# Optimization experiments

Measured on AMD Instinct MI355X. Metric: run time of the kernel, lower is better.

## Reference

```python
import jax, jax.numpy as jnp
import numpy as np

N = 50000      # num_nodes
E = 400000     # num_edges
HDIM = 256     # h_dim
H = 4          # num_heads
D = HDIM // H  # per-head dim
NEG_SLOPE = 0.2  # DGL GATConv default leaky-relu slope


def setup_inputs() -> dict:
    key = jax.random.key(0)
    ks = jax.random.split(key, 12)
    sw = 1.0 / np.sqrt(HDIM)   # fan-in scaling for fc weights
    sa = 1.0 / np.sqrt(D)      # scaling for attention vectors
    return {
        "nids": jnp.arange(N, dtype=jnp.int32),
        "edge_src": jax.random.randint(ks[0], (E,), 0, N, dtype=jnp.int32),
        "edge_dst": jax.random.randint(ks[1], (E,), 0, N, dtype=jnp.int32),
        "emb": jax.random.normal(ks[2], (N, HDIM), jnp.float32),
        "W1": jax.random.normal(ks[3], (HDIM, HDIM), jnp.float32) * sw,
        "al1": jax.random.normal(ks[4], (H, D), jnp.float32) * sa,
        "ar1": jax.random.normal(ks[5], (H, D), jnp.float32) * sa,
        "b1": jnp.zeros((HDIM,), jnp.float32),
        "W2": jax.random.normal(ks[6], (HDIM, HDIM), jnp.float32) * sw,
        "al2": jax.random.normal(ks[7], (H, D), jnp.float32) * sa,
        "ar2": jax.random.normal(ks[8], (H, D), jnp.float32) * sa,
        "b2": jnp.zeros((HDIM,), jnp.float32),
    }


def _gat_layer(x, src, dst, W, al, ar, b):
    # DGL GATConv: fc -> per-head attn logits -> edge softmax over dst -> scatter-add
    f = (x @ W).reshape(-1, H, D)                       # [N,H,D]
    el = jnp.einsum('nhd,hd->nh', f, al)                # [N,H]
    er = jnp.einsum('nhd,hd->nh', f, ar)                # [N,H]
    e = jax.nn.leaky_relu(el[src] + er[dst], NEG_SLOPE) # [E,H]
    # segment softmax over incoming edges of each dst node
    m = jax.ops.segment_max(e, dst, num_segments=N)     # [N,H] (-inf for empty)
    ex = jnp.exp(e - m[dst])                            # [E,H]
    s = jax.ops.segment_sum(ex, dst, num_segments=N)    # [N,H]
    alpha = ex / s[dst]                                 # [E,H]
    msg = alpha[:, :, None] * f[src]                    # [E,H,D]
    out = jax.ops.segment_sum(msg, dst, num_segments=N) # [N,H,D]
    return out + b.reshape(1, H, D)


def reference(nids, edge_src, edge_dst, emb, W1, al1, ar1, b1, W2, al2, ar2, b2):
    x = emb[nids]                                        # embedding lookup [N,HDIM]
    h = _gat_layer(x, edge_src, edge_dst, W1, al1, ar1, b1)  # [N,H,D]
    h = jax.nn.elu(h)
    h = h.reshape(-1, HDIM)                              # concat heads for layer 2
    out = _gat_layer(h, edge_src, edge_dst, W2, al2, ar2, b2)  # [N,H,D]
    return out  # dropout is identity at inference
```

## Files before the change

kernel.cpp:

```cpp
#include <hip/hip_runtime.h>
#include <math.h>

#define NN 50000
#define EE 400000
#define HD 256
#define NH 4
#define DH 64
#define NEG_SLOPE 0.2f
#define NTILES 3125

typedef __attribute__((ext_vector_type(8))) _Float16 f16x8;
typedef __attribute__((ext_vector_type(4))) float f32x4;

__device__ __forceinline__ float bf2f(unsigned short h) {
  return __uint_as_float(((unsigned)h) << 16);
}

__global__ void k_zero_i32(int* __restrict__ p, int n) {
  int i = blockIdx.x * blockDim.x + threadIdx.x;
  if (i < n) p[i] = 0;
}

__global__ void k_count(const int* __restrict__ dst, int* __restrict__ counts,
                        int* __restrict__ rank) {
  int e = blockIdx.x * blockDim.x + threadIdx.x;
  if (e < EE) rank[e] = atomicAdd(&counts[dst[e]], 1);
}

__global__ void k_scan1(const int* __restrict__ counts, int* __restrict__ row_ptr,
                        int* __restrict__ bsums) {
  __shared__ int sm[256];
  int i = blockIdx.x * 256 + threadIdx.x;
  int v = (i < NN) ? counts[i] : 0;
  sm[threadIdx.x] = v;
  __syncthreads();
  for (int off = 1; off < 256; off <<= 1) {
    int t = (threadIdx.x >= off) ? sm[threadIdx.x - off] : 0;
    __syncthreads();
    sm[threadIdx.x] += t;
    __syncthreads();
  }
  if (i < NN) row_ptr[i + 1] = sm[threadIdx.x];
  if (threadIdx.x == 255) bsums[blockIdx.x] = sm[255];
}

__global__ void k_scan2(int* __restrict__ bsums, int nb) {
  __shared__ int sm[256];
  int v = (threadIdx.x < nb) ? bsums[threadIdx.x] : 0;
  sm[threadIdx.x] = v;
  __syncthreads();
  for (int off = 1; off < 256; off <<= 1) {
    int t = (threadIdx.x >= off) ? sm[threadIdx.x - off] : 0;
    __syncthreads();
    sm[threadIdx.x] += t;
    __syncthreads();
  }
  if (threadIdx.x < nb) bsums[threadIdx.x] = sm[threadIdx.x] - v;
}

__global__ void k_scan3(int* __restrict__ row_ptr, const int* __restrict__ bsums) {
  int i = blockIdx.x * 256 + threadIdx.x;
  if (i < NN) row_ptr[i + 1] += bsums[blockIdx.x];
  if (blockIdx.x == 0 && threadIdx.x == 0) row_ptr[0] = 0;
}

__global__ void k_scatter(const int* __restrict__ src, const int* __restrict__ dst,
                          const int* __restrict__ row_ptr, const int* __restrict__ rank,
                          int* __restrict__ csr_src) {
  int e = blockIdx.x * blockDim.x + threadIdx.x;
  if (e < EE) csr_src[row_ptr[dst[e]] + rank[e]] = src[e];
}

__global__ __launch_bounds__(256) void k_prep_w2(const float* __restrict__ W1,
                                                 const float* __restrict__ W2,
                                                 _Float16* __restrict__ W1t,
                                                 _Float16* __restrict__ W2t) {
  int b = blockIdx.x;
  const float* W = (b < 256) ? W1 : W2;
  _Float16* Wt = (b < 256) ? W1t : W2t;
  int t = (b & 255) * 256 + threadIdx.x;
  int n = t & 255, k = t >> 8;
  float x = W[(size_t)k * 256 + n];
  size_t o = (size_t)(k >> 5) * 8192 + (size_t)((k >> 3) & 3) * 2048 + (size_t)n * 8 + (k & 7);
  Wt[o] = (_Float16)x;
}

__device__ __forceinline__ void gload_lds16(const void* g, void* l) {
  __builtin_amdgcn_global_load_lds((const __attribute__((address_space(1))) void*)g,
                                   (__attribute__((address_space(3))) void*)l, 16, 0, 0);
}

__global__ __launch_bounds__(768, 3) void k_gemm_mfma(
    const float* __restrict__ A, const int* __restrict__ idx,
    const _Float16* __restrict__ Wt,
    const float* __restrict__ al, const float* __restrict__ ar,
    __bf16* __restrict__ C, float* __restrict__ el, float* __restrict__ er) {
  __shared__ f16x8 Bs[8192];

  int tid = threadIdx.x;
  int lane = tid & 63;
  int w = tid >> 6;
  int khalf = lane >> 4;
  int l15 = lane & 15;

  for (int i = tid; i < 8192; i += 768)
    gload_lds16(Wt + (size_t)i * 8, (void*)&Bs[i]);

  float alv[16], arv[16];
#pragma unroll
  for (int nf = 0; nf < 16; ++nf) {
    alv[nf] = al[nf * 16 + l15];
    arv[nf] = ar[nf * 16 + l15];
  }

  int nt = 1;
  int tiles[2];
  tiles[0] = blockIdx.x * 12 + w;
  int t2 = 3072 + blockIdx.x;
  if (w == 0 && t2 < NTILES) { tiles[1] = t2; nt = 2; }

  __syncthreads();

  for (int it = 0; it < nt; ++it) {
    int t = tiles[it];
    int row = t * 16 + l15;
    int arow = idx ? idx[row] : row;
    const float* ap = A + (size_t)arow * HD + khalf * 8;

    f32x4 acc[16];
#pragma unroll
    for (int nf = 0; nf < 16; ++nf) acc[nf] = (f32x4){0.f, 0.f, 0.f, 0.f};

#pragma unroll 2
    for (int kb = 0; kb < 8; ++kb) {
      float xx[8];
      *(float4*)&xx[0] = *(const float4*)(ap + kb * 32);
      *(float4*)&xx[4] = *(const float4*)(ap + kb * 32 + 4);
      f16x8 ah, alo;
#pragma unroll
      for (int i = 0; i < 8; ++i) {
        _Float16 h = (_Float16)xx[i];
        ah[i] = h;
        alo[i] = (_Float16)(xx[i] - (float)h);
      }
#pragma unroll
      for (int nf = 0; nf < 16; ++nf) {
        f16x8 bv = Bs[kb * 1024 + khalf * 256 + nf * 16 + l15];
        acc[nf] = __builtin_amdgcn_mfma_f32_16x16x32_f16(ah, bv, acc[nf], 0, 0, 0);
        acc[nf] = __builtin_amdgcn_mfma_f32_16x16x32_f16(alo, bv, acc[nf], 0, 0, 0);
      }
    }

    int rowbase = t * 16 + khalf * 4;
#pragma unroll
    for (int r = 0; r < 4; ++r) {
      int row_ = rowbase + r;
      float seh[4], srh[4];
#pragma unroll
      for (int h = 0; h < 4; ++h) {
        float s1 = 0.f, s2 = 0.f;
#pragma unroll
        for (int j = 0; j < 4; ++j) {
          int nf = h * 4 + j;
          float v = acc[nf][r];
          s1 = fmaf(v, alv[nf], s1);
          s2 = fmaf(v, arv[nf], s2);
          C[(size_t)row_ * HD + nf * 16 + l15] = (__bf16)v;
        }
#pragma unroll
        for (int off = 1; off < 16; off <<= 1) {
          s1 += __shfl_xor(s1, off);
          s2 += __shfl_xor(s2, off);
        }
        seh[h] = s1;
        srh[h] = s2;
      }
      if (l15 == 0) {
        *(float4*)&el[row_ * NH] = make_float4(seh[0], seh[1], seh[2], seh[3]);
        *(float4*)&er[row_ * NH] = make_float4(srh[0], srh[1], srh[2], srh[3]);
      }
    }
  }
}

__global__ __launch_bounds__(256) void k_aggregate(const __bf16* __restrict__ f,
                                                   const float* __restrict__ el,
                                                   const float* __restrict__ er,
                                                   const int* __restrict__ row_ptr,
                                                   const int* __restrict__ csr_src,
                                                   const float* __restrict__ bias,
                                                   float* __restrict__ out, int act) {
  int node = blockIdx.x * 4 + (threadIdx.x >> 6);
  if (node >= NN) return;
  int lane = threadIdx.x & 63;
  int start = row_ptr[node];
  int deg = row_ptr[node + 1] - start;

  float ern = er[node * NH + (lane & 3)];

  int sreg[4];
  float ereg[4];
  float mloc = -INFINITY;
#pragma unroll
  for (int c = 0; c < 4; ++c) {
    int j = c * 16 + (lane >> 2);
    int s = 0;
    float e = -INFINITY;
    if (c * 16 < deg && j < deg) {
      s = csr_src[start + j];
      e = el[s * NH + (lane & 3)] + ern;
      e = (e >= 0.f) ? e : NEG_SLOPE * e;
    }
    sreg[c] = s;
    ereg[c] = e;
    mloc = fmaxf(mloc, e);
  }
  for (int j0 = 64; j0 < deg; j0 += 16) {
    int j = j0 + (lane >> 2);
    if (j < deg) {
      int s = csr_src[start + j];
      float e = el[s * NH + (lane & 3)] + ern;
      e = (e >= 0.f) ? e : NEG_SLOPE * e;
      mloc = fmaxf(mloc, e);
    }
  }
  float mm = mloc;
#pragma unroll
  for (int off = 4; off < 64; off <<= 1) mm = fmaxf(mm, __shfl_xor(mm, off));

  float vreg[4];
  float vloc = 0.f;
#pragma unroll
  for (int c = 0; c < 4; ++c) {
    float v = (ereg[c] > -INFINITY) ? __expf(ereg[c] - mm) : 0.f;
    vreg[c] = v;
    vloc += v;
  }
  for (int j0 = 64; j0 < deg; j0 += 16) {
    int j = j0 + (lane >> 2);
    if (j < deg) {
      int s = csr_src[start + j];
      float e = el[s * NH + (lane & 3)] + ern;
      e = (e >= 0.f) ? e : NEG_SLOPE * e;
      vloc += __expf(e - mm);
    }
  }
  float ss = vloc;
#pragma unroll
  for (int off = 4; off < 64; off <<= 1) ss += __shfl_xor(ss, off);

  float inv_own = (ss > 0.f) ? (1.f / ss) : 0.f;
  float areg[4];
#pragma unroll
  for (int c = 0; c < 4; ++c) areg[c] = vreg[c] * inv_own;

  int head = lane >> 4;

  float4 acc = ((const float4*)bias)[lane];
  for (int c = 0; c < 4; ++c) {
    int base = c * 16;
    if (base >= deg) break;
    int cnt = deg - base;
    cnt = (cnt > 16) ? 16 : cnt;
    for (int g = 0; g < cnt; g += 8) {
      ushort4 u[8];
      float aa[8];
#pragma unroll
      for (int jj = 0; jj < 8; ++jj) {
        int j = g + jj;
        int jc = (j < cnt) ? j : (cnt - 1);
        int srcl = jc * 4 + head;
        int s = __shfl(sreg[c], srcl);
        float a = __shfl(areg[c], srcl);
        aa[jj] = (j < cnt) ? a : 0.f;
        u[jj] = ((const ushort4*)(f + (size_t)s * HD))[lane];
      }
#pragma unroll
      for (int jj = 0; jj < 8; ++jj) {
        acc.x = fmaf(aa[jj], bf2f(u[jj].x), acc.x);
        acc.y = fmaf(aa[jj], bf2f(u[jj].y), acc.y);
        acc.z = fmaf(aa[jj], bf2f(u[jj].z), acc.z);
        acc.w = fmaf(aa[jj], bf2f(u[jj].w), acc.w);
      }
    }
  }
  if (deg > 64) {
    float mH = __shfl(mm, head);
    float sH = __shfl(ss, head);
    float erH = __shfl(ern, head);
    float invH = (sH > 0.f) ? (1.f / sH) : 0.f;
    for (int j = 64; j < deg; ++j) {
      int s = csr_src[start + j];
      float e = el[s * NH + head] + erH;
      e = (e >= 0.f) ? e : NEG_SLOPE * e;
      float a = __expf(e - mH) * invH;
      ushort4 u = ((const ushort4*)(f + (size_t)s * HD))[lane];
      acc.x = fmaf(a, bf2f(u.x), acc.x);
      acc.y = fmaf(a, bf2f(u.y), acc.y);
      acc.z = fmaf(a, bf2f(u.z), acc.z);
      acc.w = fmaf(a, bf2f(u.w), acc.w);
    }
  }

  if (act) {
    acc.x = (acc.x > 0.f) ? acc.x : __expf(acc.x) - 1.f;
    acc.y = (acc.y > 0.f) ? acc.y : __expf(acc.y) - 1.f;
    acc.z = (acc.z > 0.f) ? acc.z : __expf(acc.z) - 1.f;
    acc.w = (acc.w > 0.f) ? acc.w : __expf(acc.w) - 1.f;
  }
  ((float4*)(out + (size_t)node * HD))[lane] = acc;
}

extern "C" void kernel_launch(void* const* d_in, const int* in_sizes, int n_in,
                              void* d_out, int out_size, void* d_ws, size_t ws_size,
                              hipStream_t stream) {
  const int* nids = (const int*)d_in[0];
  const int* esrc = (const int*)d_in[1];
  const int* edst = (const int*)d_in[2];
  const float* emb = (const float*)d_in[3];
  const float* W1 = (const float*)d_in[4];
  const float* al1 = (const float*)d_in[5];
  const float* ar1 = (const float*)d_in[6];
  const float* b1 = (const float*)d_in[7];
  const float* W2 = (const float*)d_in[8];
  const float* al2 = (const float*)d_in[9];
  const float* ar2 = (const float*)d_in[10];
  const float* b2 = (const float*)d_in[11];
  float* out = (float*)d_out;

  char* w = (char*)d_ws;
  size_t off = 0;
  auto alloc = [&](size_t bytes) {
    void* p = w + off;
    off += (bytes + 255) & ~(size_t)255;
    return p;
  };
  __bf16* fbuf = (__bf16*)alloc((size_t)NN * HD * 2);
  float* el = (float*)alloc((size_t)NN * NH * 4);
  float* er = (float*)alloc((size_t)NN * NH * 4);
  int* row_ptr = (int*)alloc((size_t)(NN + 1) * 4);
  int* counts = (int*)alloc((size_t)NN * 4);
  int* rank = (int*)alloc((size_t)EE * 4);
  int* csr_src = (int*)alloc((size_t)EE * 4);
  int* bsums = (int*)alloc(1024);
  _Float16* W1t = (_Float16*)alloc((size_t)HD * HD * 2);
  _Float16* W2t = (_Float16*)alloc((size_t)HD * HD * 2);

  int nbN = (NN + 255) / 256;
  int nbE = (EE + 255) / 256;

  k_zero_i32<<<nbN, 256, 0, stream>>>(counts, NN);
  k_count<<<nbE, 256, 0, stream>>>(edst, counts, rank);
  k_scan1<<<nbN, 256, 0, stream>>>(counts, row_ptr, bsums);
  k_scan2<<<1, 256, 0, stream>>>(bsums, nbN);
  k_scan3<<<nbN, 256, 0, stream>>>(row_ptr, bsums);
  k_scatter<<<nbE, 256, 0, stream>>>(esrc, edst, row_ptr, rank, csr_src);
  k_prep_w2<<<512, 256, 0, stream>>>(W1, W2, W1t, W2t);

  int nbNode4 = (NN + 3) / 4;

  k_gemm_mfma<<<256, 768, 0, stream>>>(emb, nids, W1t, al1, ar1, fbuf, el, er);
  k_aggregate<<<nbNode4, 256, 0, stream>>>(fbuf, el, er, row_ptr, csr_src, b1, out, 1);

  k_gemm_mfma<<<256, 768, 0, stream>>>(out, nullptr, W2t, al2, ar2, fbuf, el, er);
  k_aggregate<<<nbNode4, 256, 0, stream>>>(fbuf, el, er, row_ptr, csr_src, b2, out, 0);
}
```

Before: 182.5 us.

## Split wavefront into two half-waves gathering 16-byte bf16 rows per lane

The aggregation now splits the 64-lane wavefront into two halves. Each half processes alternate edges, and each lane loads 16 bytes (8 bf16 values) instead of 8. This halves the number of gather load instructions and the per-edge loop trip count, using wider vector loads on the random row gathers. In exchange it adds a cross-half shuffle reduction of 8 accumulators, more registers, and a remapped output and bias layout.

```diff
diff --git a/kernel.cpp b/kernel.cpp
--- a/kernel.cpp
+++ b/kernel.cpp
@@ -254,61 +254,81 @@
 #pragma unroll
   for (int c = 0; c < 4; ++c) areg[c] = vreg[c] * inv_own;
 
-  int head = lane >> 4;
-
-  float4 acc = ((const float4*)bias)[lane];
+  int h = lane >> 5;
+  int l31 = lane & 31;
+  int headf = l31 >> 3;
+
+  float acc[8];
+#pragma unroll
+  for (int i = 0; i < 8; ++i) acc[i] = 0.f;
+
   for (int c = 0; c < 4; ++c) {
     int base = c * 16;
     if (base >= deg) break;
     int cnt = deg - base;
     cnt = (cnt > 16) ? 16 : cnt;
     for (int g = 0; g < cnt; g += 8) {
-      ushort4 u[8];
-      float aa[8];
-#pragma unroll
-      for (int jj = 0; jj < 8; ++jj) {
-        int j = g + jj;
+      float4 raw[4];
+      float aa[4];
+#pragma unroll
+      for (int p = 0; p < 4; ++p) {
+        int j = g + 2 * p + h;
         int jc = (j < cnt) ? j : (cnt - 1);
-        int srcl = jc * 4 + head;
+        int srcl = (jc << 2) | headf;
         int s = __shfl(sreg[c], srcl);
         float a = __shfl(areg[c], srcl);
-        aa[jj] = (j < cnt) ? a : 0.f;
-        u[jj] = ((const ushort4*)(f + (size_t)s * HD))[lane];
-      }
-#pragma unroll
-      for (int jj = 0; jj < 8; ++jj) {
-        acc.x = fmaf(aa[jj], bf2f(u[jj].x), acc.x);
-        acc.y = fmaf(aa[jj], bf2f(u[jj].y), acc.y);
-        acc.z = fmaf(aa[jj], bf2f(u[jj].z), acc.z);
-        acc.w = fmaf(aa[jj], bf2f(u[jj].w), acc.w);
+        aa[p] = (j < cnt) ? a : 0.f;
+        raw[p] = ((const float4*)(f + (size_t)s * HD))[l31];
+      }
+#pragma unroll
+      for (int p = 0; p < 4; ++p) {
+        const unsigned* u = (const unsigned*)&raw[p];
+#pragma unroll
+        for (int k = 0; k < 4; ++k) {
+          acc[2 * k] = fmaf(aa[p], __uint_as_float(u[k] << 16), acc[2 * k]);
+          acc[2 * k + 1] = fmaf(aa[p], __uint_as_float(u[k] & 0xffff0000u), acc[2 * k + 1]);
+        }
       }
     }
   }
   if (deg > 64) {
-    float mH = __shfl(mm, head);
-    float sH = __shfl(ss, head);
-    float erH = __shfl(ern, head);
+    float mH = __shfl(mm, headf);
+    float sH = __shfl(ss, headf);
+    float erH = __shfl(ern, headf);
     float invH = (sH > 0.f) ? (1.f / sH) : 0.f;
-    for (int j = 64; j < deg; ++j) {
-      int s = csr_src[start + j];
-      float e = el[s * NH + head] + erH;
+    for (int j0 = 64; j0 < deg; j0 += 2) {
+      int j = j0 + h;
+      int jc = (j < deg) ? j : (deg - 1);
+      int s = csr_src[start + jc];
+      float e = el[s * NH + headf] + erH;
       e = (e >= 0.f) ? e : NEG_SLOPE * e;
-      float a = __expf(e - mH) * invH;
-      ushort4 u = ((const ushort4*)(f + (size_t)s * HD))[lane];
-      acc.x = fmaf(a, bf2f(u.x), acc.x);
-      acc.y = fmaf(a, bf2f(u.y), acc.y);
-      acc.z = fmaf(a, bf2f(u.z), acc.z);
-      acc.w = fmaf(a, bf2f(u.w), acc.w);
-    }
-  }
-
+      float a = (j < deg) ? __expf(e - mH) * invH : 0.f;
+      float4 raw = ((const float4*)(f + (size_t)s * HD))[l31];
+      const unsigned* u = (const unsigned*)&raw;
+#pragma unroll
+      for (int k = 0; k < 4; ++k) {
+        acc[2 * k] = fmaf(a, __uint_as_float(u[k] << 16), acc[2 * k]);
+        acc[2 * k + 1] = fmaf(a, __uint_as_float(u[k] & 0xffff0000u), acc[2 * k + 1]);
+      }
+    }
+  }
+
+#pragma unroll
+  for (int i = 0; i < 8; ++i) acc[i] += __shfl_xor(acc[i], 32);
+  float4 r;
+  r.x = h ? acc[4] : acc[0];
+  r.y = h ? acc[5] : acc[1];
+  r.z = h ? acc[6] : acc[2];
+  r.w = h ? acc[7] : acc[3];
+  float4 bv = ((const float4*)bias)[2 * l31 + h];
+  r.x += bv.x; r.y += bv.y; r.z += bv.z; r.w += bv.w;
   if (act) {
-    acc.x = (acc.x > 0.f) ? acc.x : __expf(acc.x) - 1.f;
-    acc.y = (acc.y > 0.f) ? acc.y : __expf(acc.y) - 1.f;
-    acc.z = (acc.z > 0.f) ? acc.z : __expf(acc.z) - 1.f;
-    acc.w = (acc.w > 0.f) ? acc.w : __expf(acc.w) - 1.f;
-  }
-  ((float4*)(out + (size_t)node * HD))[lane] = acc;
+    r.x = (r.x > 0.f) ? r.x : __expf(r.x) - 1.f;
+    r.y = (r.y > 0.f) ? r.y : __expf(r.y) - 1.f;
+    r.z = (r.z > 0.f) ? r.z : __expf(r.z) - 1.f;
+    r.w = (r.w > 0.f) ? r.w : __expf(r.w) - 1.f;
+  }
+  ((float4*)(out + (size_t)node * HD))[2 * l31 + h] = r;
 }
 
 extern "C" void kernel_launch(void* const* d_in, const int* in_sizes, int n_in,
```

Result: slower. 191.1 us (+4.7%).

## Split aggregation into softmax and feature-sliced gather; replace scan with atomic allocation

Applied to the files above, without the earlier changes.

Replaces the three-kernel prefix scan with one atomic-allocation kernel that hands each node a contiguous CSR segment in arbitrary order. The GEMM now writes features as eight column slices of 32 values each. The fused aggregate kernel is split into a softmax kernel that writes per-edge alphas to a head-major buffer, and a gather kernel in which each block handles one feature slice over a contiguous node range, so gathered rows come from a smaller working set that can stay cache-resident. In exchange it writes and re-reads alpha and csr_src once per slice, and it adds kernel launches.

```diff
diff --git a/kernel.cpp b/kernel.cpp
--- a/kernel.cpp
+++ b/kernel.cpp
@@ -12,10 +12,6 @@
 typedef __attribute__((ext_vector_type(8))) _Float16 f16x8;
 typedef __attribute__((ext_vector_type(4))) float f32x4;
 
-__device__ __forceinline__ float bf2f(unsigned short h) {
-  return __uint_as_float(((unsigned)h) << 16);
-}
-
 __global__ void k_zero_i32(int* __restrict__ p, int n) {
   int i = blockIdx.x * blockDim.x + threadIdx.x;
   if (i < n) p[i] = 0;
@@ -27,48 +23,17 @@
   if (e < EE) rank[e] = atomicAdd(&counts[dst[e]], 1);
 }
 
-__global__ void k_scan1(const int* __restrict__ counts, int* __restrict__ row_ptr,
-                        int* __restrict__ bsums) {
-  __shared__ int sm[256];
-  int i = blockIdx.x * 256 + threadIdx.x;
-  int v = (i < NN) ? counts[i] : 0;
-  sm[threadIdx.x] = v;
-  __syncthreads();
-  for (int off = 1; off < 256; off <<= 1) {
-    int t = (threadIdx.x >= off) ? sm[threadIdx.x - off] : 0;
-    __syncthreads();
-    sm[threadIdx.x] += t;
-    __syncthreads();
-  }
-  if (i < NN) row_ptr[i + 1] = sm[threadIdx.x];
-  if (threadIdx.x == 255) bsums[blockIdx.x] = sm[255];
-}
-
-__global__ void k_scan2(int* __restrict__ bsums, int nb) {
-  __shared__ int sm[256];
-  int v = (threadIdx.x < nb) ? bsums[threadIdx.x] : 0;
-  sm[threadIdx.x] = v;
-  __syncthreads();
-  for (int off = 1; off < 256; off <<= 1) {
-    int t = (threadIdx.x >= off) ? sm[threadIdx.x - off] : 0;
-    __syncthreads();
-    sm[threadIdx.x] += t;
-    __syncthreads();
-  }
-  if (threadIdx.x < nb) bsums[threadIdx.x] = sm[threadIdx.x] - v;
-}
-
-__global__ void k_scan3(int* __restrict__ row_ptr, const int* __restrict__ bsums) {
-  int i = blockIdx.x * 256 + threadIdx.x;
-  if (i < NN) row_ptr[i + 1] += bsums[blockIdx.x];
-  if (blockIdx.x == 0 && threadIdx.x == 0) row_ptr[0] = 0;
+__global__ void k_alloc(const int* __restrict__ counts, int* __restrict__ rstart,
+                        int* __restrict__ total) {
+  int i = blockIdx.x * blockDim.x + threadIdx.x;
+  if (i < NN) rstart[i] = atomicAdd(total, counts[i]);
 }
 
 __global__ void k_scatter(const int* __restrict__ src, const int* __restrict__ dst,
-                          const int* __restrict__ row_ptr, const int* __restrict__ rank,
+                          const int* __restrict__ rstart, const int* __restrict__ rank,
                           int* __restrict__ csr_src) {
   int e = blockIdx.x * blockDim.x + threadIdx.x;
-  if (e < EE) csr_src[row_ptr[dst[e]] + rank[e]] = src[e];
+  if (e < EE) csr_src[rstart[dst[e]] + rank[e]] = src[e];
 }
 
 __global__ __launch_bounds__(256) void k_prep_w2(const float* __restrict__ W1,
@@ -94,7 +59,7 @@
     const float* __restrict__ A, const int* __restrict__ idx,
     const _Float16* __restrict__ Wt,
     const float* __restrict__ al, const float* __restrict__ ar,
-    __bf16* __restrict__ C, float* __restrict__ el, float* __restrict__ er) {
+    __bf16* __restrict__ fsl, float* __restrict__ el, float* __restrict__ er) {
   __shared__ f16x8 Bs[8192];
 
   int tid = threadIdx.x;
@@ -165,7 +130,7 @@
           float v = acc[nf][r];
           s1 = fmaf(v, alv[nf], s1);
           s2 = fmaf(v, arv[nf], s2);
-          C[(size_t)row_ * HD + nf * 16 + l15] = (__bf16)v;
+          fsl[(size_t)(nf >> 1) * NN * 32 + (size_t)row_ * 32 + (nf & 1) * 16 + l15] = (__bf16)v;
         }
 #pragma unroll
         for (int off = 1; off < 16; off <<= 1) {
@@ -183,18 +148,18 @@
   }
 }
 
-__global__ __launch_bounds__(256) void k_aggregate(const __bf16* __restrict__ f,
-                                                   const float* __restrict__ el,
-                                                   const float* __restrict__ er,
-                                                   const int* __restrict__ row_ptr,
-                                                   const int* __restrict__ csr_src,
-                                                   const float* __restrict__ bias,
-                                                   float* __restrict__ out, int act) {
+__global__ __launch_bounds__(256) void k_softmax(const float* __restrict__ el,
+                                                 const float* __restrict__ er,
+                                                 const int* __restrict__ rstart,
+                                                 const int* __restrict__ degs,
+                                                 const int* __restrict__ csr_src,
+                                                 float* __restrict__ alpha) {
   int node = blockIdx.x * 4 + (threadIdx.x >> 6);
   if (node >= NN) return;
   int lane = threadIdx.x & 63;
-  int start = row_ptr[node];
-  int deg = row_ptr[node + 1] - start;
+  int start = rstart[node];
+  int deg = degs[node];
+  if (deg == 0) return;
 
   float ern = er[node * NH + (lane & 3)];
 
@@ -250,65 +215,74 @@
   for (int off = 4; off < 64; off <<= 1) ss += __shfl_xor(ss, off);
 
   float inv_own = (ss > 0.f) ? (1.f / ss) : 0.f;
-  float areg[4];
-#pragma unroll
-  for (int c = 0; c < 4; ++c) areg[c] = vreg[c] * inv_own;
-
-  int head = lane >> 4;
-
-  float4 acc = ((const float4*)bias)[lane];
+
+#pragma unroll
   for (int c = 0; c < 4; ++c) {
-    int base = c * 16;
-    if (base >= deg) break;
-    int cnt = deg - base;
-    cnt = (cnt > 16) ? 16 : cnt;
-    for (int g = 0; g < cnt; g += 8) {
-      ushort4 u[8];
-      float aa[8];
-#pragma unroll
-      for (int jj = 0; jj < 8; ++jj) {
-        int j = g + jj;
-        int jc = (j < cnt) ? j : (cnt - 1);
-        int srcl = jc * 4 + head;
-        int s = __shfl(sreg[c], srcl);
-        float a = __shfl(areg[c], srcl);
-        aa[jj] = (j < cnt) ? a : 0.f;
-        u[jj] = ((const ushort4*)(f + (size_t)s * HD))[lane];
-      }
-#pragma unroll
-      for (int jj = 0; jj < 8; ++jj) {
-        acc.x = fmaf(aa[jj], bf2f(u[jj].x), acc.x);
-        acc.y = fmaf(aa[jj], bf2f(u[jj].y), acc.y);
-        acc.z = fmaf(aa[jj], bf2f(u[jj].z), acc.z);
-        acc.w = fmaf(aa[jj], bf2f(u[jj].w), acc.w);
-      }
-    }
-  }
-  if (deg > 64) {
-    float mH = __shfl(mm, head);
-    float sH = __shfl(ss, head);
-    float erH = __shfl(ern, head);
-    float invH = (sH > 0.f) ? (1.f / sH) : 0.f;
-    for (int j = 64; j < deg; ++j) {
+    int j = c * 16 + (lane >> 2);
+    if (c * 16 < deg && j < deg)
+      alpha[(size_t)(lane & 3) * EE + start + j] = vreg[c] * inv_own;
+  }
+  for (int j0 = 64; j0 < deg; j0 += 16) {
+    int j = j0 + (lane >> 2);
+    if (j < deg) {
       int s = csr_src[start + j];
-      float e = el[s * NH + head] + erH;
+      float e = el[s * NH + (lane & 3)] + ern;
       e = (e >= 0.f) ? e : NEG_SLOPE * e;
-      float a = __expf(e - mH) * invH;
-      ushort4 u = ((const ushort4*)(f + (size_t)s * HD))[lane];
-      acc.x = fmaf(a, bf2f(u.x), acc.x);
-      acc.y = fmaf(a, bf2f(u.y), acc.y);
-      acc.z = fmaf(a, bf2f(u.z), acc.z);
-      acc.w = fmaf(a, bf2f(u.w), acc.w);
-    }
-  }
-
-  if (act) {
-    acc.x = (acc.x > 0.f) ? acc.x : __expf(acc.x) - 1.f;
-    acc.y = (acc.y > 0.f) ? acc.y : __expf(acc.y) - 1.f;
-    acc.z = (acc.z > 0.f) ? acc.z : __expf(acc.z) - 1.f;
-    acc.w = (acc.w > 0.f) ? acc.w : __expf(acc.w) - 1.f;
-  }
-  ((float4*)(out + (size_t)node * HD))[lane] = acc;
+      alpha[(size_t)(lane & 3) * EE + start + j] = __expf(e - mm) * inv_own;
+    }
+  }
+}
+
+__global__ __launch_bounds__(256) void k_gather(const __bf16* __restrict__ fsl,
+                                                const float* __restrict__ alpha,
+                                                const int* __restrict__ rstart,
+                                                const int* __restrict__ degs,
+                                                const int* __restrict__ csr_src,
+                                                const float* __restrict__ bias,
+                                                float* __restrict__ out, int act) {
+  int b = blockIdx.x;
+  int s = b & 7;
+  int g = b >> 3;
+  int w = threadIdx.x >> 6;
+  int lane = threadIdx.x & 63;
+  int esub = lane >> 4, fl = lane & 15;
+
+  const __bf16* fbase = fsl + (size_t)s * NN * 32;
+  const float* abase = alpha + (size_t)(s >> 1) * EE;
+  float2 bv = *(const float2*)&bias[s * 32 + fl * 2];
+
+  int n0 = g * 196 + w * 49;
+  int n1 = n0 + 49;
+  if (n1 > NN) n1 = NN;
+
+  for (int node = n0; node < n1; ++node) {
+    int start = rstart[node];
+    int deg = degs[node];
+    float a0 = 0.f, a1 = 0.f;
+    for (int j0 = 0; j0 < deg; j0 += 4) {
+      int j = j0 + esub;
+      int jc = (j < deg) ? j : (deg - 1);
+      int srcn = csr_src[start + jc];
+      float a = (j < deg) ? abase[start + jc] : 0.f;
+      unsigned u = *(const unsigned*)(fbase + (size_t)srcn * 32 + fl * 2);
+      a0 = fmaf(a, __uint_as_float(u << 16), a0);
+      a1 = fmaf(a, __uint_as_float(u & 0xffff0000u), a1);
+    }
+    a0 += __shfl_xor(a0, 16);
+    a1 += __shfl_xor(a1, 16);
+    a0 += __shfl_xor(a0, 32);
+    a1 += __shfl_xor(a1, 32);
+    if (lane < 16) {
+      float2 r;
+      r.x = a0 + bv.x;
+      r.y = a1 + bv.y;
+      if (act) {
+        r.x = (r.x > 0.f) ? r.x : __expf(r.x) - 1.f;
+        r.y = (r.y > 0.f) ? r.y : __expf(r.y) - 1.f;
+      }
+      *(float2*)&out[(size_t)node * HD + s * 32 + fl * 2] = r;
+    }
+  }
 }
 
 extern "C" void kernel_launch(void* const* d_in, const int* in_sizes, int n_in,
@@ -335,33 +309,34 @@
     off += (bytes + 255) & ~(size_t)255;
     return p;
   };
-  __bf16* fbuf = (__bf16*)alloc((size_t)NN * HD * 2);
+  __bf16* fsl = (__bf16*)alloc((size_t)NN * HD * 2);
   float* el = (float*)alloc((size_t)NN * NH * 4);
   float* er = (float*)alloc((size_t)NN * NH * 4);
-  int* row_ptr = (int*)alloc((size_t)(NN + 1) * 4);
-  int* counts = (int*)alloc((size_t)NN * 4);
+  float* alpha = (float*)alloc((size_t)NH * EE * 4);
+  int* rstart = (int*)alloc((size_t)NN * 4);
+  int* counts = (int*)alloc((size_t)(NN + 8) * 4);
+  int* total = counts + NN;
   int* rank = (int*)alloc((size_t)EE * 4);
   int* csr_src = (int*)alloc((size_t)EE * 4);
-  int* bsums = (int*)alloc(1024);
   _Float16* W1t = (_Float16*)alloc((size_t)HD * HD * 2);
   _Float16* W2t = (_Float16*)alloc((size_t)HD * HD * 2);
 
-  int nbN = (NN + 255) / 256;
+  int nbN = (NN + 8 + 255) / 256;
   int nbE = (EE + 255) / 256;
 
-  k_zero_i32<<<nbN, 256, 0, stream>>>(counts, NN);
+  k_zero_i32<<<nbN, 256, 0, stream>>>(counts, NN + 8);
   k_count<<<nbE, 256, 0, stream>>>(edst, counts, rank);
-  k_scan1<<<nbN, 256, 0, stream>>>(counts, row_ptr, bsums);
-  k_scan2<<<1, 256, 0, stream>>>(bsums, nbN);
-  k_scan3<<<nbN, 256, 0, stream>>>(row_ptr, bsums);
-  k_scatter<<<nbE, 256, 0, stream>>>(esrc, edst, row_ptr, rank, csr_src);
+  k_alloc<<<(NN + 255) / 256, 256, 0, stream>>>(counts, rstart, total);
+  k_scatter<<<nbE, 256, 0, stream>>>(esrc, edst, rstart, rank, csr_src);
   k_prep_w2<<<512, 256, 0, stream>>>(W1, W2, W1t, W2t);
 
   int nbNode4 = (NN + 3) / 4;
 
-  k_gemm_mfma<<<256, 768, 0, stream>>>(emb, nids, W1t, al1, ar1, fbuf, el, er);
-  k_aggregate<<<nbNode4, 256, 0, stream>>>(fbuf, el, er, row_ptr, csr_src, b1, out, 1);
-
-  k_gemm_mfma<<<256, 768, 0, stream>>>(out, nullptr, W2t, al2, ar2, fbuf, el, er);
-  k_aggregate<<<nbNode4, 256, 0, stream>>>(fbuf, el, er, row_ptr, csr_src, b2, out, 0);
-}
+  k_gemm_mfma<<<256, 768, 0, stream>>>(emb, nids, W1t, al1, ar1, fsl, el, er);
+  k_softmax<<<nbNode4, 256, 0, stream>>>(el, er, rstart, counts, csr_src, alpha);
+  k_gather<<<2048, 256, 0, stream>>>(fsl, alpha, rstart, counts, csr_src, b1, out, 1);
+
+  k_gemm_mfma<<<256, 768, 0, stream>>>(out, nullptr, W2t, al2, ar2, fsl, el, er);
+  k_softmax<<<nbNode4, 256, 0, stream>>>(el, er, rstart, counts, csr_src, alpha);
+  k_gather<<<2048, 256, 0, stream>>>(fsl, alpha, rstart, counts, csr_src, b2, out, 0);
+}
```

Result: slower. 364.5 us (+99.7%).
